# Kernel optimization log

Hardware: AMD Instinct MI355X
Metric: run time of the kernel (lower is better)

Reference implementation:

```python
import jax, jax.numpy as jnp
import numpy as np

B, T, C, H = 4, 4096, 256, 64

def setup_inputs() -> dict:
    key = jax.random.key(0)
    k1, k2, k3, k4 = jax.random.split(key, 4)
    x = jax.random.normal(k1, (B, T, C), dtype=jnp.float32)
    # DenseSynapse weights ~ uniform(-0.1, 0.1); randn spec approximated faithfully in math, init dist irrelevant to correctness
    Wk = jax.random.uniform(k2, (C, H), minval=-0.1, maxval=0.1, dtype=jnp.float32)
    Wq = jax.random.uniform(k3, (C, H), minval=-0.1, maxval=0.1, dtype=jnp.float32)
    Wv = jax.random.uniform(k4, (C, H), minval=-0.1, maxval=0.1, dtype=jnp.float32)
    return {"x": x, "Wk": Wk, "Wq": Wq, "Wv": Wv}

def reference(x, Wk, Wq, Wv):
    Bq, Tq, Cq = x.shape
    # linear projections (DenseSynapse.advance_state with Rscale=1, no bias): x @ W
    k = jnp.einsum('btc,ch->bth', x, Wk)
    q = jnp.einsum('btc,ch->bth', x, Wq)
    v = jnp.einsum('btc,ch->bth', x, Wv)
    # scores scaled by C**-0.5 (n_embd, as in source)
    wei = jnp.einsum('bqh,bkh->bqk', q, k) * (Cq ** -0.5)
    mask = jnp.tril(jnp.ones((Tq, Tq), dtype=bool))
    wei = jnp.where(mask, wei, -jnp.inf)
    wei = jax.nn.softmax(wei, axis=-1)
    # dropout deterministic (eval) in reference
    out = jnp.einsum('bqk,bkh->bqh', wei, v)
    return out
```

## Files before the change

kernel.cpp:

```cpp
#include <hip/hip_runtime.h>
#include <hip/hip_bf16.h>
#include <math.h>

#define Bb   4
#define T    4096
#define Cc   256
#define Hh   64
#define BT   (Bb*T)
#define CPB  144

using f32x4  = __attribute__((ext_vector_type(4))) float;
using f32x16 = __attribute__((ext_vector_type(16))) float;
using short8 = __attribute__((ext_vector_type(8))) short;
using int4v  = __attribute__((ext_vector_type(4))) int;

__device__ __forceinline__ float fexp2(float x) {
    return __builtin_amdgcn_exp2f(x);
}
__device__ __forceinline__ ushort f2bf(float f) {
    unsigned u = __builtin_bit_cast(unsigned, f);
    return (ushort)((u + 0x8000u) >> 16);
}
__device__ __forceinline__ float bf2f(ushort u) {
    return __builtin_bit_cast(float, (unsigned)u << 16);
}
__device__ __forceinline__ int swzb(int row, int cb) { return (row<<7) + (cb ^ ((row&7)<<4)); }
__device__ __forceinline__ int swzx(int row, int cb) { return (row<<9) + (cb ^ ((row&7)<<4)); }
__device__ __forceinline__ int chunk_prefix(int qt) {
    const int a = qt >> 2, r = qt & 3;
    return 2*a*(a+1) + r*(a+1);
}

#define GLOAD16(g, l) __builtin_amdgcn_global_load_lds( \
    (const __attribute__((address_space(1))) unsigned*)(g), \
    (__attribute__((address_space(3))) unsigned*)(l), 16, 0, 0)

__global__ __launch_bounds__(256) void wtrans(
    const float* __restrict__ Wq, const float* __restrict__ Wk,
    const float* __restrict__ Wv, ushort* __restrict__ WtG)
{
    __shared__ float wl[256][65];
    const int t = threadIdx.x;
    const int m = blockIdx.x;
    const float* W = (m==0) ? Wq : (m==1) ? Wk : Wv;
    const float scale = (m==0) ? 0.09016844005556021f : 1.0f;
    for (int idx = t; idx < 4096; idx += 256) {
        const float4 v4 = ((const float4*)W)[idx];
        const int c = idx >> 4;
        const int h = (idx & 15) * 4;
        wl[c][h+0]=v4.x*scale; wl[c][h+1]=v4.y*scale;
        wl[c][h+2]=v4.z*scale; wl[c][h+3]=v4.w*scale;
    }
    __syncthreads();
    const int h  = t & 63;
    const int n  = m*64 + h;
    const int c0 = (t >> 6) * 64;
    for (int c = c0; c < c0 + 64; c += 4) {
        ushort4 o;
        o.x=f2bf(wl[c+0][h]); o.y=f2bf(wl[c+1][h]);
        o.z=f2bf(wl[c+2][h]); o.w=f2bf(wl[c+3][h]);
        *(ushort4*)((char*)WtG + n*512 + ((c*2) ^ ((n&7)<<4))) = o;
    }
}

__global__ __launch_bounds__(256) void proj_mfma(
    const float* __restrict__ x, const ushort* __restrict__ WtG,
    ushort* __restrict__ qo, ushort* __restrict__ ko, ushort* __restrict__ vtG)
{
    __shared__ ushort xls[64*256];
    __shared__ ushort wls[192*256];
    const int t = threadIdx.x, w = t>>6, lane = t&63, g = lane>>4, ln = lane&15;
    const int blk = blockIdx.x;
    const long rowbase = (long)blk * 64;
    const int b    = blk >> 6;
    const int trow = (blk & 63) * 64;

    {
        const char* src = (const char*)WtG + (long)lane*16;
        for (int c = w; c < 96; c += 4)
            GLOAD16(src + c*1024, (char*)wls + c*1024);
    }
    for (int j = 0; j < 16; ++j) {
        const int idx = t + j*256;
        const int row = idx >> 6;
        const int c4  = (idx & 63) * 4;
        const float4 xv = ((const float4*)x)[(rowbase + row)*64 + (c4>>2)];
        ushort4 o; o.x=f2bf(xv.x); o.y=f2bf(xv.y); o.z=f2bf(xv.z); o.w=f2bf(xv.w);
        *(ushort4*)((char*)xls + swzx(row, c4*2)) = o;
    }
    __syncthreads();

    short8 xf[8];
    #pragma unroll
    for (int ks = 0; ks < 8; ++ks)
        xf[ks] = *(const short8*)((const char*)xls + swzx(w*16+ln, ks*64 + g*16));

    #pragma unroll
    for (int nt = 0; nt < 12; ++nt) {
        f32x4 acc = (f32x4){0.f,0.f,0.f,0.f};
        #pragma unroll
        for (int ks = 0; ks < 8; ++ks) {
            const short8 wf = *(const short8*)((const char*)wls + swzx(nt*16+ln, ks*64 + g*16));
            acc = (nt < 8) ? __builtin_amdgcn_mfma_f32_16x16x32_bf16(wf, xf[ks], acc, 0,0,0)
                           : __builtin_amdgcn_mfma_f32_16x16x32_bf16(xf[ks], wf, acc, 0,0,0);
        }
        ushort4 o; o.x=f2bf(acc[0]); o.y=f2bf(acc[1]); o.z=f2bf(acc[2]); o.w=f2bf(acc[3]);
        if (nt < 4) {
            *(ushort4*)(qo + (rowbase + w*16 + ln)*64 + nt*16 + g*4) = o;
        } else if (nt < 8) {
            *(ushort4*)(ko + (rowbase + w*16 + ln)*64 + (nt-4)*16 + g*4) = o;
        } else {
            *(ushort4*)(vtG + ((long)b*64 + (nt-8)*16 + ln)*T + trow + w*16 + g*4) = o;
        }
    }
}

__global__ __launch_bounds__(256) void attn_mfma(
    const ushort* __restrict__ q, const ushort* __restrict__ k,
    const ushort* __restrict__ vt,
    ushort* __restrict__ part_o, float* __restrict__ part_ml)
{
    __shared__ ushort kls[2][4096];
    __shared__ ushort vtls[2][4096];

    const int bid = blockIdx.x;
    const int b   = bid & 3;
    const int w2  = (CPB - 1) - (bid >> 2);
    int qt = 0, c = 0;
    {
        int acc = 0;
        for (int qq = 0; qq < 32; ++qq) {
            const int n = (qq + 4) >> 2;
            if (w2 < acc + n) { qt = qq; c = w2 - acc; break; }
            acc += n;
        }
    }
    const int kt0   = c * 8;
    const int ktend = min(2*qt + 1, kt0 + 7);
    const int ntile = ktend - kt0 + 1;
    const int pid   = b*CPB + chunk_prefix(qt) + c;

    const int t = threadIdx.x, w = t>>6, lane = t&63;
    const int l5 = lane & 31, g5 = lane >> 5;
    const int lrow = lane >> 3;
    const int lc16 = ((lane & 7) ^ lrow) * 16;
    const char* kbase = (const char*)k  + ((long)b*T)*128;
    const char* vbase = (const char*)vt + ((long)b*64)*(long)T*2;

    #define STAGE(bufi, ktile) do { \
        _Pragma("unroll") for (int j = 0; j < 2; ++j) { const int ci = w*2 + j; \
            GLOAD16(kbase + (long)(ktile)*8192 + ci*1024 + lrow*128 + lc16, \
                    (char*)kls[bufi] + ci*1024); \
            GLOAD16(vbase + ((long)(8*ci + lrow))*8192 + (long)(ktile)*128 + lc16, \
                    (char*)vtls[bufi] + ci*1024); \
        } } while(0)

    const int qmin = qt*128 + w*32;
    const int qrow = qmin + l5;
    short8 qf[4];
    {
        const ushort* qp = q + ((long)(b*T + qrow))*64;
        #pragma unroll
        for (int hs = 0; hs < 4; ++hs)
            qf[hs] = *(const short8*)(qp + hs*16 + g5*8);
    }

    f32x16 o0, o1;
    #pragma unroll
    for (int i = 0; i < 16; ++i) { o0[i] = 0.f; o1[i] = 0.f; }
    float mrun = -INFINITY, lpart = 0.f;

    STAGE(0, kt0);
    for (int it = 0; it < ntile; ++it) {
        const int kt  = kt0 + it;
        const int cur = it & 1;
        __syncthreads();
        if (it + 1 < ntile) STAGE(cur^1, kt + 1);
        if (kt*64 > qmin + 31) continue;

        f32x16 s0, s1;
        #pragma unroll
        for (int i = 0; i < 16; ++i) { s0[i] = 0.f; s1[i] = 0.f; }
        __builtin_amdgcn_s_setprio(1);
        #pragma unroll
        for (int hs = 0; hs < 4; ++hs) {
            const short8 kf0 = *(const short8*)((const char*)kls[cur] + swzb(l5,    hs*32 + g5*16));
            s0 = __builtin_amdgcn_mfma_f32_32x32x16_bf16(kf0, qf[hs], s0, 0, 0, 0);
            const short8 kf1 = *(const short8*)((const char*)kls[cur] + swzb(32+l5, hs*32 + g5*16));
            s1 = __builtin_amdgcn_mfma_f32_32x32x16_bf16(kf1, qf[hs], s1, 0, 0, 0);
        }
        __builtin_amdgcn_s_setprio(0);

        if (kt*64 + 63 > qmin) {
            #pragma unroll
            for (int reg = 0; reg < 16; ++reg) {
                const int kl = (reg&3) + 8*(reg>>2) + 4*g5;
                if (kt*64 + kl      > qrow) s0[reg] = -INFINITY;
                if (kt*64 + 32 + kl > qrow) s1[reg] = -INFINITY;
            }
        }

        bool ok = true;
        #pragma unroll
        for (int r = 0; r < 16; ++r) {
            ok &= (s0[r] <= mrun + 11.5f);
            ok &= (s1[r] <= mrun + 11.5f);
        }
        if (!__all(ok)) {
            float mt = s0[0];
            #pragma unroll
            for (int r = 1; r < 16; ++r) mt = fmaxf(mt, s0[r]);
            #pragma unroll
            for (int r = 0; r < 16; ++r) mt = fmaxf(mt, s1[r]);
            mt = fmaxf(mt, __shfl_xor(mt, 32));
            const float mn = fmaxf(mrun, mt);
            const float corr = fexp2(mrun - mn);
            lpart *= corr;
            #pragma unroll
            for (int r = 0; r < 16; ++r) { o0[r] *= corr; o1[r] *= corr; }
            mrun = mn;
        }

        unsigned u0[8], u1[8];
        #pragma unroll
        for (int i = 0; i < 8; ++i) {
            const float pa = fexp2(s0[2*i+0] - mrun);
            const float pb = fexp2(s0[2*i+1] - mrun);
            lpart += pa + pb;
            u0[i] = (unsigned)f2bf(pa) | ((unsigned)f2bf(pb) << 16);
            const float pc = fexp2(s1[2*i+0] - mrun);
            const float pd = fexp2(s1[2*i+1] - mrun);
            lpart += pc + pd;
            u1[i] = (unsigned)f2bf(pc) | ((unsigned)f2bf(pd) << 16);
        }
        unsigned x0[8], x1[8];
        #pragma unroll
        for (int i = 0; i < 8; ++i) {
            x0[i] = (unsigned)__shfl_xor((int)u0[i], 32);
            x1[i] = (unsigned)__shfl_xor((int)u1[i], 32);
        }
        int4v pw[4];
        #pragma unroll
        for (int s = 0; s < 2; ++s) {
            pw[s].x   = g5 ? (int)x0[4*s+2] : (int)u0[4*s+0];
            pw[s].y   = g5 ? (int)x0[4*s+3] : (int)u0[4*s+1];
            pw[s].z   = g5 ? (int)u0[4*s+2] : (int)x0[4*s+0];
            pw[s].w   = g5 ? (int)u0[4*s+3] : (int)x0[4*s+1];
            pw[2+s].x = g5 ? (int)x1[4*s+2] : (int)u1[4*s+0];
            pw[2+s].y = g5 ? (int)x1[4*s+3] : (int)u1[4*s+1];
            pw[2+s].z = g5 ? (int)u1[4*s+2] : (int)x1[4*s+0];
            pw[2+s].w = g5 ? (int)u1[4*s+3] : (int)x1[4*s+1];
        }

        __builtin_amdgcn_s_setprio(1);
        #pragma unroll
        for (int ks2 = 0; ks2 < 4; ++ks2) {
            const short8 pa = __builtin_bit_cast(short8, pw[ks2]);
            const short8 vf0 = *(const short8*)((const char*)vtls[cur] + swzb(l5,    ks2*32 + g5*16));
            o0 = __builtin_amdgcn_mfma_f32_32x32x16_bf16(vf0, pa, o0, 0, 0, 0);
            const short8 vf1 = *(const short8*)((const char*)vtls[cur] + swzb(32+l5, ks2*32 + g5*16));
            o1 = __builtin_amdgcn_mfma_f32_32x32x16_bf16(vf1, pa, o1, 0, 0, 0);
        }
        __builtin_amdgcn_s_setprio(0);
    }
    #undef STAGE

    const float ltot = lpart + __shfl_xor(lpart, 32);
    if (g5 == 0) {
        part_ml[((long)pid*128 + w*32 + l5)*2 + 0] = mrun;
        part_ml[((long)pid*128 + w*32 + l5)*2 + 1] = ltot;
    }
    ushort* po = part_o + (long)pid*8192 + (w*32 + l5)*64;
    #pragma unroll
    for (int rq = 0; rq < 4; ++rq) {
        ushort4 a;
        a.x = f2bf(o0[4*rq+0]); a.y = f2bf(o0[4*rq+1]);
        a.z = f2bf(o0[4*rq+2]); a.w = f2bf(o0[4*rq+3]);
        *(ushort4*)(po + 8*rq + 4*g5) = a;
        ushort4 bq;
        bq.x = f2bf(o1[4*rq+0]); bq.y = f2bf(o1[4*rq+1]);
        bq.z = f2bf(o1[4*rq+2]); bq.w = f2bf(o1[4*rq+3]);
        *(ushort4*)(po + 32 + 8*rq + 4*g5) = bq;
    }
}

__global__ __launch_bounds__(128) void attn_merge(
    const ushort* __restrict__ part_o, const float* __restrict__ part_ml,
    float* __restrict__ out)
{
    const int bid = blockIdx.x;
    const int hh = bid & 1;
    const int qt = (bid >> 1) & 31;
    const int b  = bid >> 6;
    const int t  = threadIdx.x;
    const int nseg = (qt + 4) >> 2;
    const int base = b*CPB + chunk_prefix(qt);

    float ms[8], ls[8];
    float mstar = -INFINITY;
    for (int s = 0; s < nseg; ++s) {
        ms[s] = part_ml[((long)(base+s)*128 + t)*2 + 0];
        ls[s] = part_ml[((long)(base+s)*128 + t)*2 + 1];
        mstar = fmaxf(mstar, ms[s]);
    }
    float acc[32];
    #pragma unroll
    for (int h = 0; h < 32; ++h) acc[h] = 0.f;
    float lsum = 0.f;
    for (int s = 0; s < nseg; ++s) {
        const float wgt = fexp2(ms[s] - mstar);
        lsum += ls[s] * wgt;
        const short8* po = (const short8*)(part_o + (long)(base+s)*8192 + t*64 + hh*32);
        #pragma unroll
        for (int j = 0; j < 4; ++j) {
            const short8 v8 = po[j];
            #pragma unroll
            for (int e = 0; e < 8; ++e)
                acc[j*8+e] += wgt * bf2f((ushort)v8[e]);
        }
    }
    const float inv = 1.f / lsum;
    float* op = out + ((long)b*T + qt*128 + t)*64 + hh*32;
    #pragma unroll
    for (int j = 0; j < 8; ++j)
        ((float4*)op)[j] = make_float4(acc[4*j+0]*inv, acc[4*j+1]*inv,
                                       acc[4*j+2]*inv, acc[4*j+3]*inv);
}

extern "C" void kernel_launch(void* const* d_in, const int* in_sizes, int n_in,
                              void* d_out, int out_size, void* d_ws, size_t ws_size,
                              hipStream_t stream)
{
    const float* x  = (const float*)d_in[0];
    const float* Wk = (const float*)d_in[1];
    const float* Wq = (const float*)d_in[2];
    const float* Wv = (const float*)d_in[3];

    char* w8 = (char*)d_ws;
    ushort* qb      = (ushort*)(w8);
    ushort* kb      = (ushort*)(w8 + (2l<<20));
    ushort* vt      = (ushort*)(w8 + (4l<<20));
    ushort* Wt      = (ushort*)(w8 + (6l<<20));
    ushort* part_o  = (ushort*)(w8 + (7l<<20));
    float*  part_ml = (float*) (w8 + (17l<<20));

    wtrans    <<<3,        256, 0, stream>>>(Wq, Wk, Wv, Wt);
    proj_mfma <<<BT/64,    256, 0, stream>>>(x, Wt, qb, kb, vt);
    attn_mfma <<<Bb*CPB,   256, 0, stream>>>(qb, kb, vt, part_o, part_ml);
    attn_merge<<<Bb*32*2,  128, 0, stream>>>(part_o, part_ml, (float*)d_out);
}
```

Before: 66.53 us.

## Halve attention key-chunk size, drop LDS weight staging, widen merge grid

Attention split-K chunks shrink from 8 to 4 key tiles, so blocks per batch rise from 144 to 272. This spreads the causal workload over more CUs with shorter per-block runs. Projection weights are now read straight from global/L1 without swizzle instead of being staged into LDS, which cuts LDS usage and should raise occupancy. The merge kernel is reorganised with more blocks and fewer outputs per thread; it now has more partials to combine, and the partial buffers grow.

```diff
diff --git a/kernel.cpp b/kernel.cpp
--- a/kernel.cpp
+++ b/kernel.cpp
@@ -7,7 +7,7 @@
 #define Cc   256
 #define Hh   64
 #define BT   (Bb*T)
-#define CPB  144
+#define CPB  272
 
 using f32x4  = __attribute__((ext_vector_type(4))) float;
 using f32x16 = __attribute__((ext_vector_type(16))) float;
@@ -27,8 +27,8 @@
 __device__ __forceinline__ int swzb(int row, int cb) { return (row<<7) + (cb ^ ((row&7)<<4)); }
 __device__ __forceinline__ int swzx(int row, int cb) { return (row<<9) + (cb ^ ((row&7)<<4)); }
 __device__ __forceinline__ int chunk_prefix(int qt) {
-    const int a = qt >> 2, r = qt & 3;
-    return 2*a*(a+1) + r*(a+1);
+    const int a = qt >> 1;
+    return (qt & 1) ? (a+1)*(a+1) : a*(a+1);
 }
 
 #define GLOAD16(g, l) __builtin_amdgcn_global_load_lds( \
@@ -59,7 +59,7 @@
         ushort4 o;
         o.x=f2bf(wl[c+0][h]); o.y=f2bf(wl[c+1][h]);
         o.z=f2bf(wl[c+2][h]); o.w=f2bf(wl[c+3][h]);
-        *(ushort4*)((char*)WtG + n*512 + ((c*2) ^ ((n&7)<<4))) = o;
+        *(ushort4*)(WtG + n*256 + c) = o;
     }
 }
 
@@ -68,18 +68,12 @@
     ushort* __restrict__ qo, ushort* __restrict__ ko, ushort* __restrict__ vtG)
 {
     __shared__ ushort xls[64*256];
-    __shared__ ushort wls[192*256];
     const int t = threadIdx.x, w = t>>6, lane = t&63, g = lane>>4, ln = lane&15;
     const int blk = blockIdx.x;
     const long rowbase = (long)blk * 64;
     const int b    = blk >> 6;
     const int trow = (blk & 63) * 64;
 
-    {
-        const char* src = (const char*)WtG + (long)lane*16;
-        for (int c = w; c < 96; c += 4)
-            GLOAD16(src + c*1024, (char*)wls + c*1024);
-    }
     for (int j = 0; j < 16; ++j) {
         const int idx = t + j*256;
         const int row = idx >> 6;
@@ -97,10 +91,11 @@
 
     #pragma unroll
     for (int nt = 0; nt < 12; ++nt) {
+        const ushort* wrow = WtG + (nt*16 + ln)*256 + g*8;
         f32x4 acc = (f32x4){0.f,0.f,0.f,0.f};
         #pragma unroll
         for (int ks = 0; ks < 8; ++ks) {
-            const short8 wf = *(const short8*)((const char*)wls + swzx(nt*16+ln, ks*64 + g*16));
+            const short8 wf = *(const short8*)(wrow + ks*32);
             acc = (nt < 8) ? __builtin_amdgcn_mfma_f32_16x16x32_bf16(wf, xf[ks], acc, 0,0,0)
                            : __builtin_amdgcn_mfma_f32_16x16x32_bf16(xf[ks], wf, acc, 0,0,0);
         }
@@ -130,13 +125,13 @@
     {
         int acc = 0;
         for (int qq = 0; qq < 32; ++qq) {
-            const int n = (qq + 4) >> 2;
+            const int n = (qq + 2) >> 1;
             if (w2 < acc + n) { qt = qq; c = w2 - acc; break; }
             acc += n;
         }
     }
-    const int kt0   = c * 8;
-    const int ktend = min(2*qt + 1, kt0 + 7);
+    const int kt0   = c * 4;
+    const int ktend = min(2*qt + 1, kt0 + 3);
     const int ntile = ktend - kt0 + 1;
     const int pid   = b*CPB + chunk_prefix(qt) + c;
 
@@ -289,40 +284,40 @@
     float* __restrict__ out)
 {
     const int bid = blockIdx.x;
-    const int hh = bid & 1;
-    const int qt = (bid >> 1) & 31;
-    const int b  = bid >> 6;
-    const int t  = threadIdx.x;
-    const int nseg = (qt + 4) >> 2;
+    const int qs  = bid & 3;
+    const int qt  = (bid >> 2) & 31;
+    const int b   = bid >> 7;
+    const int t = threadIdx.x, w = t >> 6, lane = t & 63;
+    const int ql = qs*32 + w*16 + (lane >> 2);
+    const int h0 = (lane & 3) * 16;
+    const int nseg = (qt + 2) >> 1;
     const int base = b*CPB + chunk_prefix(qt);
 
-    float ms[8], ls[8];
     float mstar = -INFINITY;
     for (int s = 0; s < nseg; ++s) {
-        ms[s] = part_ml[((long)(base+s)*128 + t)*2 + 0];
-        ls[s] = part_ml[((long)(base+s)*128 + t)*2 + 1];
-        mstar = fmaxf(mstar, ms[s]);
-    }
-    float acc[32];
-    #pragma unroll
-    for (int h = 0; h < 32; ++h) acc[h] = 0.f;
+        const float2 ml = *(const float2*)(part_ml + ((long)(base+s)*128 + ql)*2);
+        mstar = fmaxf(mstar, ml.x);
+    }
+    float acc[16];
+    #pragma unroll
+    for (int i = 0; i < 16; ++i) acc[i] = 0.f;
     float lsum = 0.f;
     for (int s = 0; s < nseg; ++s) {
-        const float wgt = fexp2(ms[s] - mstar);
-        lsum += ls[s] * wgt;
-        const short8* po = (const short8*)(part_o + (long)(base+s)*8192 + t*64 + hh*32);
-        #pragma unroll
-        for (int j = 0; j < 4; ++j) {
-            const short8 v8 = po[j];
-            #pragma unroll
-            for (int e = 0; e < 8; ++e)
-                acc[j*8+e] += wgt * bf2f((ushort)v8[e]);
+        const float2 ml = *(const float2*)(part_ml + ((long)(base+s)*128 + ql)*2);
+        const float wgt = fexp2(ml.x - mstar);
+        lsum += ml.y * wgt;
+        const short8* po = (const short8*)(part_o + (long)(base+s)*8192 + ql*64 + h0);
+        const short8 a = po[0], c8 = po[1];
+        #pragma unroll
+        for (int e = 0; e < 8; ++e) {
+            acc[e]   += wgt * bf2f((ushort)a[e]);
+            acc[8+e] += wgt * bf2f((ushort)c8[e]);
         }
     }
     const float inv = 1.f / lsum;
-    float* op = out + ((long)b*T + qt*128 + t)*64 + hh*32;
-    #pragma unroll
-    for (int j = 0; j < 8; ++j)
+    float* op = out + ((long)b*T + qt*128 + ql)*64 + h0;
+    #pragma unroll
+    for (int j = 0; j < 4; ++j)
         ((float4*)op)[j] = make_float4(acc[4*j+0]*inv, acc[4*j+1]*inv,
                                        acc[4*j+2]*inv, acc[4*j+3]*inv);
 }
@@ -342,10 +337,10 @@
     ushort* vt      = (ushort*)(w8 + (4l<<20));
     ushort* Wt      = (ushort*)(w8 + (6l<<20));
     ushort* part_o  = (ushort*)(w8 + (7l<<20));
-    float*  part_ml = (float*) (w8 + (17l<<20));
-
-    wtrans    <<<3,        256, 0, stream>>>(Wq, Wk, Wv, Wt);
-    proj_mfma <<<BT/64,    256, 0, stream>>>(x, Wt, qb, kb, vt);
-    attn_mfma <<<Bb*CPB,   256, 0, stream>>>(qb, kb, vt, part_o, part_ml);
-    attn_merge<<<Bb*32*2,  128, 0, stream>>>(part_o, part_ml, (float*)d_out);
-}
+    float*  part_ml = (float*) (w8 + (25l<<20));
+
+    wtrans    <<<3,         256, 0, stream>>>(Wq, Wk, Wv, Wt);
+    proj_mfma <<<BT/64,     256, 0, stream>>>(x, Wt, qb, kb, vt);
+    attn_mfma <<<Bb*CPB,    256, 0, stream>>>(qb, kb, vt, part_o, part_ml);
+    attn_merge<<<Bb*32*4,   128, 0, stream>>>(part_o, part_ml, (float*)d_out);
+}
```

After: 71.28 us. 7.1% more time.
